# Kernel optimization log

Measured on AMD Instinct MI355X. Metric: run time of the kernel, lower is better.

Reference implementation:

```python
import jax, jax.numpy as jnp
import numpy as np

B, L, E, H = 2, 2048, 2048, 16
HD = E // H  # 128


def build_rope(length, head_dim, base=10000.0):
    # [L, head_dim//2, 2] with [..., 0]=sin, [..., 1]=cos (matches apply_rope indexing)
    half = head_dim // 2
    inv_freq = 1.0 / (base ** (jnp.arange(half, dtype=jnp.float32) * 2.0 / head_dim))
    ang = jnp.arange(length, dtype=jnp.float32)[:, None] * inv_freq[None, :]  # [L, half]
    return jnp.stack([jnp.sin(ang), jnp.cos(ang)], axis=-1)  # [L, half, 2]


def apply_rope(x, rope):
    # x: [B, L, H, D]; rope: [L, D//2, 2] (sin, cos)
    b, l, h, d = x.shape
    sin = rope[:, :, 0].reshape(1, l, 1, d // 2)
    cos = rope[:, :, 1].reshape(1, l, 1, d // 2)
    xr = x.reshape(b, l, h, d // 2, 2)
    q0, q1 = xr[..., 0], xr[..., 1]
    out = jnp.stack([q0 * cos - q1 * sin, q1 * cos + q0 * sin], axis=-1)
    return out.reshape(b, l, h, d)


def setup_inputs() -> dict:
    key = jax.random.key(0)
    k1, k2, k3 = jax.random.split(key, 3)
    x = jax.random.normal(k1, (B, L, E), dtype=jnp.float32)
    w_attn = jax.random.normal(k2, (3 * E, E), dtype=jnp.float32) * (E ** -0.5)
    w_proj = jax.random.normal(k3, (E, E), dtype=jnp.float32) * (E ** -0.5)
    rope = build_rope(L, HD)
    return {"x": x, "rope": rope, "w_attn": w_attn, "w_proj": w_proj}


def reference(x, rope, w_attn, w_proj):
    b, l, e = x.shape
    h, hd = H, HD
    qkv = jnp.einsum('ble,fe->blf', x, w_attn)  # [B, L, 3E]
    q, k, v = jnp.split(qkv, 3, axis=-1)
    q = apply_rope(q.reshape(b, l, h, hd), rope)
    k = apply_rope(k.reshape(b, l, h, hd), rope)
    v = v.reshape(b, l, h, hd)
    # causal SDPA, scale 1/sqrt(head_dim)
    scale = 1.0 / np.sqrt(hd).astype(np.float32)
    scores = jnp.einsum('bqhd,bkhd->bhqk', q, k) * scale
    causal = jnp.tril(jnp.ones((l, l), dtype=bool))
    scores = jnp.where(causal[None, None], scores, jnp.finfo(scores.dtype).min)
    att = jax.nn.softmax(scores, axis=-1)
    y = jnp.einsum('bhqk,bkhd->bqhd', att, v).reshape(b, l, e)
    return jnp.einsum('ble,fe->blf', y, w_proj)
```

## Files before the change

kernel.cpp:

```cpp
#include <hip/hip_runtime.h>
#include <math.h>

#define BATCH 2
#define LSEQ  2048
#define EMB   2048
#define NH    16
#define HD    128

typedef __attribute__((ext_vector_type(8))) short bf16x8;
typedef __attribute__((ext_vector_type(8))) unsigned short u16x8;
typedef __attribute__((ext_vector_type(4))) float f32x4;

static __device__ __forceinline__ unsigned short f2bf(float f) {
    unsigned u = __float_as_uint(f);
    u += 0x7fffu + ((u >> 16) & 1u);
    return (unsigned short)(u >> 16);
}

static __device__ __forceinline__ void load_lds16(const void* g, void* l) {
    __builtin_amdgcn_global_load_lds(
        (const __attribute__((address_space(1))) void*)g,
        (__attribute__((address_space(3))) void*)l, 16, 0, 0);
}

#define N1 (BATCH * LSEQ * EMB)
#define N2 (3 * EMB * EMB)
#define N3 (EMB * EMB)

__global__ __launch_bounds__(256) void cast_bf16_kernel(
    const float* __restrict__ x, const float* __restrict__ wa,
    const float* __restrict__ wp,
    unsigned short* __restrict__ xb, unsigned short* __restrict__ wab,
    unsigned short* __restrict__ wpb)
{
    size_t i4 = ((size_t)blockIdx.x * 256 + threadIdx.x) * 4;
    const float* src;
    unsigned short* dst;
    size_t off;
    if (i4 < (size_t)N1) { src = x; dst = xb; off = i4; }
    else if (i4 < (size_t)N1 + N2) { src = wa; dst = wab; off = i4 - N1; }
    else { src = wp; dst = wpb; off = i4 - N1 - N2; }
    float4 f = *(const float4*)(src + off);
    ushort4 u;
    u.x = f2bf(f.x); u.y = f2bf(f.y); u.z = f2bf(f.z); u.w = f2bf(f.w);
    *(ushort4*)(dst + off) = u;
}

template<int NI>
__global__ __launch_bounds__(512, 2) void gemm_bt_bf16(
    const unsigned short* __restrict__ A, const unsigned short* __restrict__ B,
    const float* __restrict__ rope,
    float* __restrict__ C,
    unsigned short* __restrict__ qo, unsigned short* __restrict__ ko,
    unsigned short* __restrict__ vo,
    int M, int N, int K, int mode)
{
    __shared__ __align__(16) unsigned short As[2][256 * 64];
    __shared__ __align__(16) unsigned short Bs[2][NI * 64 * 64];

    const int tid = threadIdx.x;
    const int lane = tid & 63;
    const int w = tid >> 6;
    const int m = lane & 15;
    const int g = lane >> 4;
    const int wr = w >> 2;
    const int wc = w & 3;
    const int sw = m & 7;

    const int nwgx = gridDim.x;
    const int lin = blockIdx.y * nwgx + blockIdx.x;
    const int cpx = (nwgx * gridDim.y) >> 3;
    const int swz = (lin & 7) * cpx + (lin >> 3);
    const int bm = (swz / nwgx) * 256;
    const int bn = (swz % nwgx) * (NI * 64);

    auto stage_half = [&](int buf, int k0, int h) {
        const bool isA = (h < 2);
        const unsigned short* S = isA ? A : B;
        const int rbase = isA ? ((h & 1) * 128) : ((h - 2) * 128);
        unsigned short* L = isA ? &As[buf][rbase * 64] : &Bs[buf][(h - 2) * 128 * 64];
        const size_t gb = isA ? (size_t)bm : (size_t)bn;
#pragma unroll
        for (int i = 0; i < 2; i++) {
            const int idx = i * 512 + tid;
            const int row = idx >> 3;
            const int c = (idx & 7) ^ (row & 7);
            load_lds16(S + (gb + rbase + row) * (size_t)K + k0 + c * 8, L + idx * 8);
        }
    };

    f32x4 acc[8][NI];
#pragma unroll
    for (int mi = 0; mi < 8; mi++)
#pragma unroll
        for (int ni = 0; ni < NI; ni++) acc[mi][ni] = (f32x4){0.f, 0.f, 0.f, 0.f};

    const int nt = K >> 6;
    const int NH_HALF = 2 + NI / 2;

#pragma unroll
    for (int h = 0; h < 4; h++)
        if (h < NH_HALF) stage_half(0, 0, h);
    asm volatile("s_waitcnt vmcnt(0)" ::: "memory");
    __builtin_amdgcn_s_barrier();

    for (int t = 0; t < nt; t++) {
        const int rd = t & 1;
        const int wrn = rd ^ 1;
        const int k1 = (t + 1) * 64;
        const unsigned short* Ac = As[rd];
        const unsigned short* Bc = Bs[rd];
        const bool pre = (t + 1 < nt);

        bf16x8 bfv[NI][2];

#pragma unroll
        for (int p = 0; p < 4; p++) {
            bf16x8 af[2][2];
#pragma unroll
            for (int mi2 = 0; mi2 < 2; mi2++) {
                const int row = wr * 128 + (p * 2 + mi2) * 16 + m;
#pragma unroll
                for (int kc = 0; kc < 2; kc++)
                    af[mi2][kc] = *(const bf16x8*)&Ac[(row * 8 + ((kc * 4 + g) ^ sw)) * 8];
            }
            if (p == 0) {
#pragma unroll
                for (int ni = 0; ni < NI; ni++) {
                    const int row = wc * (NI * 16) + ni * 16 + m;
#pragma unroll
                    for (int kc = 0; kc < 2; kc++)
                        bfv[ni][kc] = *(const bf16x8*)&Bc[(row * 8 + ((kc * 4 + g) ^ sw)) * 8];
                }
            }
            if (pre) {
                if (p == 0) { stage_half(wrn, k1, 0); stage_half(wrn, k1, 1); }
                if (p == 1) { stage_half(wrn, k1, 2); if (NI == 4) stage_half(wrn, k1, 3); }
            }

            __builtin_amdgcn_s_barrier();
            asm volatile("s_waitcnt lgkmcnt(0)" ::: "memory");
            __builtin_amdgcn_s_setprio(1);
#pragma unroll
            for (int mi2 = 0; mi2 < 2; mi2++)
#pragma unroll
                for (int ni = 0; ni < NI; ni++)
#pragma unroll
                    for (int kc = 0; kc < 2; kc++)
                        acc[p * 2 + mi2][ni] = __builtin_amdgcn_mfma_f32_16x16x32_bf16(
                            af[mi2][kc], bfv[ni][kc], acc[p * 2 + mi2][ni], 0, 0, 0);
            __builtin_amdgcn_s_setprio(0);
            if (p == 3) {
                asm volatile("s_waitcnt vmcnt(0)" ::: "memory");
            }
            __builtin_amdgcn_s_barrier();
        }
    }

#pragma unroll
    for (int mi = 0; mi < 8; mi++) {
#pragma unroll
        for (int ni = 0; ni < NI; ni++) {
            const int col = bn + wc * (NI * 16) + ni * 16 + m;
            if (mode == 0) {
#pragma unroll
                for (int r = 0; r < 4; r++) {
                    const int row = bm + wr * 128 + mi * 16 + g * 4 + r;
                    C[(size_t)row * N + col] = acc[mi][ni][r];
                }
            } else {
                const int which = col >> 11;
                const int e = col & 2047;
                const int h = e >> 7;
                const int d = e & 127;
                if (which < 2) {
                    unsigned short* dst = (which == 0) ? qo : ko;
                    const int t2 = ((d >> 1) << 1);
#pragma unroll
                    for (int r = 0; r < 4; r++) {
                        const int row = bm + wr * 128 + mi * 16 + g * 4 + r;
                        const int b = row >> 11;
                        const int l = row & 2047;
                        float val = acc[mi][ni][r];
                        const float prt = __shfl_xor(val, 1);
                        const float2 sc = *(const float2*)(rope + (size_t)l * HD + t2);
                        val = (m & 1) ? fmaf(val, sc.y, prt * sc.x)
                                      : fmaf(val, sc.y, -prt * sc.x);
                        dst[(((size_t)(b * NH + h)) * LSEQ + l) * HD + d] = f2bf(val);
                    }
                } else {
                    const int l0 = bm + wr * 128 + mi * 16 + g * 4;
                    const int b = l0 >> 11;
                    const int l = l0 & 2047;
                    ushort4 vv;
                    vv.x = f2bf(acc[mi][ni][0]);
                    vv.y = f2bf(acc[mi][ni][1]);
                    vv.z = f2bf(acc[mi][ni][2]);
                    vv.w = f2bf(acc[mi][ni][3]);
                    *(ushort4*)(vo + (((size_t)(b * NH + h)) * HD + d) * LSEQ + l) = vv;
                }
            }
        }
    }
}

__global__ __launch_bounds__(256) void gemm_bt_128(
    const unsigned short* __restrict__ A, const unsigned short* __restrict__ B,
    float* __restrict__ C, int M, int N, int K)
{
    __shared__ unsigned short As[128 * 64];
    __shared__ unsigned short Bs[128 * 64];

    const int tid = threadIdx.x;
    const int lane = tid & 63;
    const int w = tid >> 6;
    const int m = lane & 15;
    const int g = lane >> 4;
    const int wm = (w & 1) * 64;
    const int wn = (w >> 1) * 64;

    const int nwgx = gridDim.x;
    const int lin = blockIdx.y * nwgx + blockIdx.x;
    const int cpx = (nwgx * gridDim.y) >> 3;
    const int swz = (lin & 7) * cpx + (lin >> 3);
    const int bm = (swz / nwgx) * 128;
    const int bn = (swz % nwgx) * 128;

    f32x4 acc[4][4];
#pragma unroll
    for (int mi = 0; mi < 4; mi++)
#pragma unroll
        for (int ni = 0; ni < 4; ni++) acc[mi][ni] = (f32x4){0.f, 0.f, 0.f, 0.f};

    for (int k0 = 0; k0 < K; k0 += 64) {
        __syncthreads();
#pragma unroll
        for (int i = 0; i < 4; i++) {
            const int idx = i * 256 + tid;
            const int row = idx >> 3;
            const int c = (idx & 7) ^ (row & 7);
            load_lds16(A + (size_t)(bm + row) * K + k0 + c * 8, &As[idx * 8]);
            load_lds16(B + (size_t)(bn + row) * K + k0 + c * 8, &Bs[idx * 8]);
        }
        __syncthreads();

#pragma unroll
        for (int kc = 0; kc < 2; kc++) {
            bf16x8 af[4], bfv[4];
#pragma unroll
            for (int mi = 0; mi < 4; mi++) {
                const int row = wm + mi * 16 + m;
                af[mi] = *(const bf16x8*)&As[(row * 8 + ((kc * 4 + g) ^ (m & 7))) * 8];
            }
#pragma unroll
            for (int ni = 0; ni < 4; ni++) {
                const int row = wn + ni * 16 + m;
                bfv[ni] = *(const bf16x8*)&Bs[(row * 8 + ((kc * 4 + g) ^ (m & 7))) * 8];
            }
#pragma unroll
            for (int mi = 0; mi < 4; mi++)
#pragma unroll
                for (int ni = 0; ni < 4; ni++)
                    acc[mi][ni] = __builtin_amdgcn_mfma_f32_16x16x32_bf16(
                        af[mi], bfv[ni], acc[mi][ni], 0, 0, 0);
        }
    }

#pragma unroll
    for (int mi = 0; mi < 4; mi++) {
#pragma unroll
        for (int ni = 0; ni < 4; ni++) {
            const int col = bn + wn + ni * 16 + m;
#pragma unroll
            for (int r = 0; r < 4; r++) {
                const int row = bm + wm + mi * 16 + g * 4 + r;
                C[(size_t)row * N + col] = acc[mi][ni][r];
            }
        }
    }
}

#define PTILES 32
#define PS_STR 68

__global__ __launch_bounds__(256) void attn_kernel(
    const unsigned short* __restrict__ q, const unsigned short* __restrict__ k,
    const unsigned short* __restrict__ vT, unsigned short* __restrict__ y)
{
    __shared__ __align__(16) unsigned short Ks[2][64 * 128];
    __shared__ __align__(16) unsigned short Vs[2][64 * 128];
    __shared__ __align__(16) unsigned short Ps[64 * PS_STR];

    const int tid = threadIdx.x;
    const int lane = tid & 63;
    const int w = tid >> 6;
    const int m = lane & 15;
    const int g = lane >> 4;
    const int bh = blockIdx.x;
    const int qt = PTILES - 1 - blockIdx.y;
    const int q0 = qt * 64;
    const size_t base = (size_t)bh * LSEQ * HD;
    const float scale = 0.08838834764831845f;
    const int bB = bh / NH;
    const int hh = bh % NH;
    const int sw = m & 7;

    auto stage = [&](int buf, int kb0) {
        const unsigned short* ksrc = k + base + (size_t)kb0 * HD;
#pragma unroll
        for (int i = 0; i < 4; i++) {
            const int idx = i * 256 + tid;
            const int row = idx >> 4;
            const int c = (idx & 15) ^ (row & 7);
            load_lds16(ksrc + (size_t)row * HD + c * 8, &Ks[buf][idx * 8]);
        }
#pragma unroll
        for (int i = 0; i < 4; i++) {
            const int idx = i * 256 + tid;
            const int d = idx >> 3;
            const int c = (idx & 7) ^ (d & 7);
            load_lds16(vT + base + (size_t)d * LSEQ + kb0 + c * 8, &Vs[buf][idx * 8]);
        }
    };

    bf16x8 aq[4];
    {
        const unsigned short* qrow = q + base + (size_t)(q0 + w * 16 + m) * HD;
#pragma unroll
        for (int kc = 0; kc < 4; kc++)
            aq[kc] = *(const bf16x8*)(qrow + kc * 32 + g * 8);
    }

    f32x4 o[8];
#pragma unroll
    for (int i = 0; i < 8; i++) o[i] = (f32x4){0.f, 0.f, 0.f, 0.f};
    float mprev[4], lsum[4];
#pragma unroll
    for (int r = 0; r < 4; r++) { mprev[r] = -1e30f; lsum[r] = 0.f; }

    stage(0, 0);
    int cur = 0;

    for (int kt = 0; kt <= qt; kt++) {
        const int k0 = kt * 64;

        __syncthreads();

        if (kt < qt) stage(cur ^ 1, k0 + 64);

        const unsigned short* Kc = Ks[cur];
        const unsigned short* Vc = Vs[cur];

        f32x4 s[4];
#pragma unroll
        for (int n = 0; n < 4; n++) {
            f32x4 acc = (f32x4){0.f, 0.f, 0.f, 0.f};
#pragma unroll
            for (int kc = 0; kc < 4; kc++) {
                const int row = n * 16 + m;
                bf16x8 bk = *(const bf16x8*)&Kc[(row * 16 + ((kc * 4 + g) ^ sw)) * 8];
                acc = __builtin_amdgcn_mfma_f32_16x16x32_bf16(aq[kc], bk, acc, 0, 0, 0);
            }
            s[n] = acc;
        }

        const int rowg = q0 + w * 16 + g * 4;
        if (kt == qt) {
#pragma unroll
            for (int n = 0; n < 4; n++) {
                const int col = k0 + n * 16 + m;
#pragma unroll
                for (int r = 0; r < 4; r++) {
                    const float val = s[n][r] * scale;
                    s[n][r] = (col <= rowg + r) ? val : -1e30f;
                }
            }
        } else {
#pragma unroll
            for (int n = 0; n < 4; n++)
#pragma unroll
                for (int r = 0; r < 4; r++) s[n][r] *= scale;
        }

        float al[4];
#pragma unroll
        for (int r = 0; r < 4; r++) {
            float v0 = fmaxf(fmaxf(s[0][r], s[1][r]), fmaxf(s[2][r], s[3][r]));
            v0 = fmaxf(v0, __shfl_xor(v0, 1));
            v0 = fmaxf(v0, __shfl_xor(v0, 2));
            v0 = fmaxf(v0, __shfl_xor(v0, 4));
            v0 = fmaxf(v0, __shfl_xor(v0, 8));
            const float mn = fmaxf(mprev[r], v0);
            al[r] = __expf(mprev[r] - mn);
            mprev[r] = mn;
        }
#pragma unroll
        for (int r = 0; r < 4; r++) {
            float sum = 0.f;
#pragma unroll
            for (int n = 0; n < 4; n++) {
                const float p = __expf(s[n][r] - mprev[r]);
                sum += p;
                Ps[(w * 16 + g * 4 + r) * PS_STR + n * 16 + m] = f2bf(p);
            }
            sum += __shfl_xor(sum, 1);
            sum += __shfl_xor(sum, 2);
            sum += __shfl_xor(sum, 4);
            sum += __shfl_xor(sum, 8);
            lsum[r] = lsum[r] * al[r] + sum;
        }

#pragma unroll
        for (int dc = 0; dc < 8; dc++)
#pragma unroll
            for (int r = 0; r < 4; r++) o[dc][r] *= al[r];

        bf16x8 ap[2];
#pragma unroll
        for (int kk = 0; kk < 2; kk++)
            ap[kk] = *(const bf16x8*)&Ps[(w * 16 + m) * PS_STR + kk * 32 + g * 8];
#pragma unroll
        for (int dc = 0; dc < 8; dc++) {
#pragma unroll
            for (int kk = 0; kk < 2; kk++) {
                const int row = dc * 16 + m;
                bf16x8 bv = *(const bf16x8*)&Vc[(row * 8 + ((kk * 4 + g) ^ sw)) * 8];
                o[dc] = __builtin_amdgcn_mfma_f32_16x16x32_bf16(ap[kk], bv, o[dc], 0, 0, 0);
            }
        }

        cur ^= 1;
    }

#pragma unroll
    for (int r = 0; r < 4; r++) {
        const float inv = 1.f / lsum[r];
        const int lrow = q0 + w * 16 + g * 4 + r;
        unsigned short* dst = y + (((size_t)bB * LSEQ + lrow) * NH + hh) * HD;
#pragma unroll
        for (int dc = 0; dc < 8; dc++)
            dst[dc * 16 + m] = f2bf(o[dc][r] * inv);
    }
}

extern "C" void kernel_launch(void* const* d_in, const int* in_sizes, int n_in,
                              void* d_out, int out_size, void* d_ws, size_t ws_size,
                              hipStream_t stream) {
    const float* x      = (const float*)d_in[0];
    const float* rope   = (const float*)d_in[1];
    const float* w_attn = (const float*)d_in[2];
    const float* w_proj = (const float*)d_in[3];
    float* out = (float*)d_out;
    unsigned short* ws = (unsigned short*)d_ws;

    const size_t per = (size_t)BATCH * NH * LSEQ * HD;
    unsigned short* qb  = ws;
    unsigned short* kb  = ws + per;
    unsigned short* vb  = ws + 2 * per;
    unsigned short* yb  = ws + 3 * per;
    unsigned short* xb  = ws + 4 * per;
    unsigned short* wab = xb + (size_t)N1;
    unsigned short* wpb = wab + (size_t)N2;

    const int M = BATCH * LSEQ;

    const int cast_blocks = (N1 + N2 + N3) / 4 / 256;
    cast_bf16_kernel<<<cast_blocks, 256, 0, stream>>>(x, w_attn, w_proj, xb, wab, wpb);

    dim3 g1(3 * EMB / 256, M / 256);
    gemm_bt_bf16<4><<<g1, 512, 0, stream>>>(xb, wab, rope, nullptr, qb, kb, vb,
                                            M, 3 * EMB, EMB, 1);

    dim3 ga(BATCH * NH, PTILES);
    attn_kernel<<<ga, 256, 0, stream>>>(qb, kb, vb, yb);

    dim3 g2(EMB / 128, M / 128);
    gemm_bt_128<<<g2, 256, 0, stream>>>(yb, wpb, out, M, EMB, EMB);
}
```

Baseline: 402.6 us.

## Enlarge attention query tile to 128 rows with 8 waves sharing K/V stages

The attention kernel now handles 128 query rows per block with 512 threads, so each staged 64-key K/V tile is reused by eight waves instead of four. This halves the global-to-LDS traffic per query row. The kernel also sets wave priority around the MFMA sections and writes P to LDS in two 32-column halves with a smaller stride. In exchange it launches fewer, larger blocks, which hurts load balance across CUs. The lower waves also compute a fully masked final key tile, which is wasted work.

```diff
diff --git a/kernel.cpp b/kernel.cpp
--- a/kernel.cpp
+++ b/kernel.cpp
@@ -280,16 +280,16 @@
     }
 }
 
-#define PTILES 32
-#define PS_STR 68
-
-__global__ __launch_bounds__(256) void attn_kernel(
+#define QTILES 16
+#define PS_STR 40
+
+__global__ __launch_bounds__(512) void attn_kernel(
     const unsigned short* __restrict__ q, const unsigned short* __restrict__ k,
     const unsigned short* __restrict__ vT, unsigned short* __restrict__ y)
 {
     __shared__ __align__(16) unsigned short Ks[2][64 * 128];
-    __shared__ __align__(16) unsigned short Vs[2][64 * 128];
-    __shared__ __align__(16) unsigned short Ps[64 * PS_STR];
+    __shared__ __align__(16) unsigned short Vs[2][128 * 64];
+    __shared__ __align__(16) unsigned short Ps[128 * PS_STR];
 
     const int tid = threadIdx.x;
     const int lane = tid & 63;
@@ -297,8 +297,8 @@
     const int m = lane & 15;
     const int g = lane >> 4;
     const int bh = blockIdx.x;
-    const int qt = PTILES - 1 - blockIdx.y;
-    const int q0 = qt * 64;
+    const int qt = QTILES - 1 - blockIdx.y;
+    const int q0 = qt * 128;
     const size_t base = (size_t)bh * LSEQ * HD;
     const float scale = 0.08838834764831845f;
     const int bB = bh / NH;
@@ -308,15 +308,15 @@
     auto stage = [&](int buf, int kb0) {
         const unsigned short* ksrc = k + base + (size_t)kb0 * HD;
 #pragma unroll
-        for (int i = 0; i < 4; i++) {
-            const int idx = i * 256 + tid;
+        for (int i = 0; i < 2; i++) {
+            const int idx = i * 512 + tid;
             const int row = idx >> 4;
             const int c = (idx & 15) ^ (row & 7);
             load_lds16(ksrc + (size_t)row * HD + c * 8, &Ks[buf][idx * 8]);
         }
 #pragma unroll
-        for (int i = 0; i < 4; i++) {
-            const int idx = i * 256 + tid;
+        for (int i = 0; i < 2; i++) {
+            const int idx = i * 512 + tid;
             const int d = idx >> 3;
             const int c = (idx & 7) ^ (d & 7);
             load_lds16(vT + base + (size_t)d * LSEQ + kb0 + c * 8, &Vs[buf][idx * 8]);
@@ -340,18 +340,20 @@
 
     stage(0, 0);
     int cur = 0;
-
-    for (int kt = 0; kt <= qt; kt++) {
+    const int nt = 2 * qt + 2;
+
+    for (int kt = 0; kt < nt; kt++) {
         const int k0 = kt * 64;
 
         __syncthreads();
 
-        if (kt < qt) stage(cur ^ 1, k0 + 64);
+        if (kt + 1 < nt) stage(cur ^ 1, k0 + 64);
 
         const unsigned short* Kc = Ks[cur];
         const unsigned short* Vc = Vs[cur];
 
         f32x4 s[4];
+        __builtin_amdgcn_s_setprio(1);
 #pragma unroll
         for (int n = 0; n < 4; n++) {
             f32x4 acc = (f32x4){0.f, 0.f, 0.f, 0.f};
@@ -363,9 +365,10 @@
             }
             s[n] = acc;
         }
+        __builtin_amdgcn_s_setprio(0);
 
         const int rowg = q0 + w * 16 + g * 4;
-        if (kt == qt) {
+        if (kt >= 2 * qt) {
 #pragma unroll
             for (int n = 0; n < 4; n++) {
                 const int col = k0 + n * 16 + m;
@@ -399,9 +402,8 @@
             float sum = 0.f;
 #pragma unroll
             for (int n = 0; n < 4; n++) {
-                const float p = __expf(s[n][r] - mprev[r]);
-                sum += p;
-                Ps[(w * 16 + g * 4 + r) * PS_STR + n * 16 + m] = f2bf(p);
+                s[n][r] = __expf(s[n][r] - mprev[r]);
+                sum += s[n][r];
             }
             sum += __shfl_xor(sum, 1);
             sum += __shfl_xor(sum, 2);
@@ -415,18 +417,23 @@
 #pragma unroll
             for (int r = 0; r < 4; r++) o[dc][r] *= al[r];
 
-        bf16x8 ap[2];
-#pragma unroll
-        for (int kk = 0; kk < 2; kk++)
-            ap[kk] = *(const bf16x8*)&Ps[(w * 16 + m) * PS_STR + kk * 32 + g * 8];
-#pragma unroll
-        for (int dc = 0; dc < 8; dc++) {
-#pragma unroll
-            for (int kk = 0; kk < 2; kk++) {
+#pragma unroll
+        for (int kk = 0; kk < 2; kk++) {
+#pragma unroll
+            for (int r = 0; r < 4; r++)
+#pragma unroll
+                for (int n2 = 0; n2 < 2; n2++)
+                    Ps[(w * 16 + g * 4 + r) * PS_STR + n2 * 16 + m] =
+                        f2bf(s[kk * 2 + n2][r]);
+            bf16x8 ap = *(const bf16x8*)&Ps[(w * 16 + m) * PS_STR + g * 8];
+            __builtin_amdgcn_s_setprio(1);
+#pragma unroll
+            for (int dc = 0; dc < 8; dc++) {
                 const int row = dc * 16 + m;
                 bf16x8 bv = *(const bf16x8*)&Vc[(row * 8 + ((kk * 4 + g) ^ sw)) * 8];
-                o[dc] = __builtin_amdgcn_mfma_f32_16x16x32_bf16(ap[kk], bv, o[dc], 0, 0, 0);
-            }
+                o[dc] = __builtin_amdgcn_mfma_f32_16x16x32_bf16(ap, bv, o[dc], 0, 0, 0);
+            }
+            __builtin_amdgcn_s_setprio(0);
         }
 
         cur ^= 1;
@@ -471,8 +478,8 @@
     gemm_bt_bf16<4><<<g1, 512, 0, stream>>>(xb, wab, rope, nullptr, qb, kb, vb,
                                             M, 3 * EMB, EMB, 1);
 
-    dim3 ga(BATCH * NH, PTILES);
-    attn_kernel<<<ga, 256, 0, stream>>>(qb, kb, vb, yb);
+    dim3 ga(BATCH * NH, QTILES);
+    attn_kernel<<<ga, 512, 0, stream>>>(qb, kb, vb, yb);
 
     dim3 g2(EMB / 128, M / 128);
     gemm_bt_128<<<g2, 256, 0, stream>>>(yb, wpb, out, M, EMB, EMB);
```

New measurement: 412.9 us. +2.5%, slower.
